# Kernel tuning notes

Hardware: AMD Instinct MI355X
Metric: run time of the kernel (lower is better)

## Reference

```python
import jax, jax.numpy as jnp
import numpy as np

HIDDEN_DIM = 128
NUM_HEADS = 4
B, S = 16, 1024
NEG = -1e9
EPS = 1e-5


def setup_inputs() -> dict:
    key = jax.random.key(0)
    ks = jax.random.split(key, 6)
    D, H = HIDDEN_DIM, NUM_HEADS
    x = jax.random.normal(ks[0], (B, S, D), dtype=jnp.float32)
    edge_type_matrix = jax.random.randint(ks[1], (S, S), 0, 5, dtype=jnp.int64)
    scale = 0.02
    W_in = jax.random.normal(ks[2], (H, 3 * D, D), dtype=jnp.float32) * scale   # per-head in_proj_weight
    b_in = jax.random.normal(ks[3], (H, 3 * D), dtype=jnp.float32) * scale      # per-head in_proj_bias
    W_out = jax.random.normal(ks[4], (H, D, D), dtype=jnp.float32) * scale      # per-head out_proj.weight
    b_out = jax.random.normal(ks[5], (H, D), dtype=jnp.float32) * scale         # per-head out_proj.bias
    return {"x": x, "edge_type_matrix": edge_type_matrix,
            "W_in": W_in, "b_in": b_in, "W_out": W_out, "b_out": b_out}


def reference(x, edge_type_matrix, W_in, b_in, W_out, b_out):
    Bx, Sx, D = x.shape
    H = W_in.shape[0]
    # F.layer_norm(x, x.size()[1:]): normalize jointly over (S, D), no affine
    mu = jnp.mean(x, axis=(1, 2), keepdims=True)
    var = jnp.mean(jnp.square(x - mu), axis=(1, 2), keepdims=True)
    xn = (x - mu) / jnp.sqrt(var + EPS)
    # all heads' qkv in one contraction: [b,h,s,3D]
    qkv = jnp.einsum('bsd,hed->bhse', xn, W_in) + b_in[None, :, None, :]
    q, k, v = jnp.split(qkv, 3, axis=-1)                      # each [b,h,s,D]
    scores = jnp.einsum('bhsd,bhtd->bhst', q, k) / jnp.sqrt(jnp.float32(D))
    # additive mask per head: 0 where edge_type == head_id(1..H), else -1e9
    head_ids = jnp.arange(1, H + 1, dtype=edge_type_matrix.dtype)
    mask = jnp.where(edge_type_matrix[None, :, :] == head_ids[:, None, None],
                     jnp.float32(0.0), jnp.float32(NEG))       # [h,s,s]
    attn = jax.nn.softmax(scores + mask[None], axis=-1)
    ctx = jnp.einsum('bhst,bhtd->bhsd', attn, v)
    # torch out_proj: ctx @ W.T + b
    out_h = jnp.einsum('bhsd,hed->bhse', ctx, W_out) + b_out[None, :, None, :]
    # dropout p=0.05 is identity in eval mode; concat heads on feature dim
    out = jnp.transpose(out_h, (0, 2, 1, 3)).reshape(Bx, Sx, H * D)
    return out


if __name__ == '__main__':
    inp = setup_inputs()
    y = reference(**inp)
    print(y.shape)
```

## Files before the change

kernel.cpp:

```cpp
#include <hip/hip_runtime.h>
#include <math.h>

static constexpr int Dh = 128;
static constexpr int NH = 4;
static constexpr int NB = 16;
static constexpr int SS = 1024;
static constexpr float NEGF = -1e9f;
static constexpr float SCALE = 0.08838834764831843f;

typedef short s16x8 __attribute__((ext_vector_type(8)));
typedef short s16x4 __attribute__((ext_vector_type(4)));
typedef float f32x4 __attribute__((ext_vector_type(4)));

#define MFMA32(a, b, c) __builtin_amdgcn_mfma_f32_16x16x32_bf16(a, b, c, 0, 0, 0)
#define MFMA16(a, b, c) __builtin_amdgcn_mfma_f32_16x16x16bf16_1k(a, b, c, 0, 0, 0)

#define GL2LDS16(g, l)                                                                   \
    __builtin_amdgcn_global_load_lds((const __attribute__((address_space(1))) void*)(g), \
                                     (__attribute__((address_space(3))) void*)(l), 16, 0, 0)

__device__ inline ushort f2bf(float f) {
    union { float f; unsigned u; } v; v.f = f;
    unsigned r = v.u + 0x7FFFu + ((v.u >> 16) & 1u);
    return (ushort)(r >> 16);
}

__global__ __launch_bounds__(256) void ln_mask_kernel(const float* __restrict__ x,
                                                      float* __restrict__ part,
                                                      const int* __restrict__ edge,
                                                      unsigned long long* __restrict__ mbit,
                                                      const float* __restrict__ w_in,
                                                      ushort* __restrict__ wb) {
    const int b = blockIdx.x >> 4, p = blockIdx.x & 15;
    const int tid = threadIdx.x;
    const float4* xb4 = (const float4*)(x + (size_t)b * SS * Dh) + p * 2048;
    float s = 0.f, ss = 0.f;
    for (int i = tid; i < 2048; i += 256) {
        float4 v = xb4[i];
        s  += v.x + v.y + v.z + v.w;
        ss += v.x * v.x + v.y * v.y + v.z * v.z + v.w * v.w;
    }
    __shared__ float r1[256], r2[256];
    r1[tid] = s; r2[tid] = ss;
    __syncthreads();
    for (int off = 128; off > 0; off >>= 1) {
        if (tid < off) { r1[tid] += r1[tid + off]; r2[tid] += r2[tid + off]; }
        __syncthreads();
    }
    if (tid == 0) { part[blockIdx.x * 2] = r1[0]; part[blockIdx.x * 2 + 1] = r2[0]; }

    if (blockIdx.x < 64) {
        const int idx = blockIdx.x * 256 + tid;
        const int sr = idx >> 4, w = idx & 15;
        const int4* ep = (const int4*)(edge + (size_t)sr * SS + w * 64);
        unsigned long long m0 = 0, m1 = 0, m2 = 0, m3 = 0;
        #pragma unroll
        for (int j = 0; j < 16; ++j) {
            int4 e = ep[j];
            const int base = j * 4;
            m0 |= (e.x == 1) ? (1ull << (base + 0)) : 0ull;
            m1 |= (e.x == 2) ? (1ull << (base + 0)) : 0ull;
            m2 |= (e.x == 3) ? (1ull << (base + 0)) : 0ull;
            m3 |= (e.x == 4) ? (1ull << (base + 0)) : 0ull;
            m0 |= (e.y == 1) ? (1ull << (base + 1)) : 0ull;
            m1 |= (e.y == 2) ? (1ull << (base + 1)) : 0ull;
            m2 |= (e.y == 3) ? (1ull << (base + 1)) : 0ull;
            m3 |= (e.y == 4) ? (1ull << (base + 1)) : 0ull;
            m0 |= (e.z == 1) ? (1ull << (base + 2)) : 0ull;
            m1 |= (e.z == 2) ? (1ull << (base + 2)) : 0ull;
            m2 |= (e.z == 3) ? (1ull << (base + 2)) : 0ull;
            m3 |= (e.z == 4) ? (1ull << (base + 2)) : 0ull;
            m0 |= (e.w == 1) ? (1ull << (base + 3)) : 0ull;
            m1 |= (e.w == 2) ? (1ull << (base + 3)) : 0ull;
            m2 |= (e.w == 3) ? (1ull << (base + 3)) : 0ull;
            m3 |= (e.w == 4) ? (1ull << (base + 3)) : 0ull;
        }
        mbit[((size_t)0 * SS + sr) * 16 + w] = m0;
        mbit[((size_t)1 * SS + sr) * 16 + w] = m1;
        mbit[((size_t)2 * SS + sr) * 16 + w] = m2;
        mbit[((size_t)3 * SS + sr) * 16 + w] = m3;
    } else if (blockIdx.x < 160) {
        const int slot = (blockIdx.x - 64) * 256 + tid;
        const float4* sp = (const float4*)w_in + (size_t)slot * 2;
        float4 a = sp[0], c = sp[1];
        s16x8 pk;
        pk[0] = (short)f2bf(a.x); pk[1] = (short)f2bf(a.y);
        pk[2] = (short)f2bf(a.z); pk[3] = (short)f2bf(a.w);
        pk[4] = (short)f2bf(c.x); pk[5] = (short)f2bf(c.y);
        pk[6] = (short)f2bf(c.z); pk[7] = (short)f2bf(c.w);
        *(s16x8*)(wb + (size_t)slot * 8) = pk;
    }
}

__global__ __launch_bounds__(256) void xcast_kernel(const float* __restrict__ x,
                                                    const float* __restrict__ part,
                                                    ushort* __restrict__ xb) {
    const int b = blockIdx.x >> 6;
    float s = 0.f, ss = 0.f;
    #pragma unroll
    for (int p = 0; p < 16; ++p) { s += part[(b * 16 + p) * 2]; ss += part[(b * 16 + p) * 2 + 1]; }
    const float invN = 1.0f / (float)(SS * Dh);
    const float mu = s * invN;
    const float rstd = 1.0f / sqrtf(ss * invN - mu * mu + 1e-5f);
    const size_t base = ((size_t)blockIdx.x * 256 + threadIdx.x) * 8;
    float4 v0 = *(const float4*)(x + base);
    float4 v1 = *(const float4*)(x + base + 4);
    s16x8 pk;
    pk[0] = (short)f2bf((v0.x - mu) * rstd); pk[1] = (short)f2bf((v0.y - mu) * rstd);
    pk[2] = (short)f2bf((v0.z - mu) * rstd); pk[3] = (short)f2bf((v0.w - mu) * rstd);
    pk[4] = (short)f2bf((v1.x - mu) * rstd); pk[5] = (short)f2bf((v1.y - mu) * rstd);
    pk[6] = (short)f2bf((v1.z - mu) * rstd); pk[7] = (short)f2bf((v1.w - mu) * rstd);
    *(s16x8*)(xb + base) = pk;
}

__global__ __launch_bounds__(256) void qkv_mfma_kernel(const ushort* __restrict__ xb,
                                                       const ushort* __restrict__ wb,
                                                       const float* __restrict__ bias,
                                                       ushort* __restrict__ qo,
                                                       ushort* __restrict__ ko,
                                                       ushort* __restrict__ vto) {
    __shared__ ushort smem[2 * 128 * 72];
    ushort* As = smem;
    ushort* Bs = smem + 128 * 72;
    ushort* Rs = smem;
    const int tid = threadIdx.x, wave = tid >> 6, lane = tid & 63;
    const int lrow = lane & 15, quad = lane >> 4;
    const int wm = wave & 1, wn = wave >> 1;
    const int col0 = blockIdx.x * 128;
    const int row0 = blockIdx.y * 128;
    const int bb = row0 >> 10;

    f32x4 acc[4][4];
    #pragma unroll
    for (int mi = 0; mi < 4; ++mi)
        #pragma unroll
        for (int ni = 0; ni < 4; ++ni) acc[mi][ni] = (f32x4){0.f, 0.f, 0.f, 0.f};

    for (int kk = 0; kk < 128; kk += 64) {
        if (kk) __syncthreads();
        #pragma unroll
        for (int p = 0; p < 4; ++p) {
            int slot = p * 256 + tid;
            int r = slot >> 3, c8 = (slot & 7) * 8;
            *(s16x8*)&As[r * 72 + c8] = *(const s16x8*)(xb + (size_t)(row0 + r) * Dh + kk + c8);
            *(s16x8*)&Bs[r * 72 + c8] = *(const s16x8*)(wb + (size_t)(col0 + r) * Dh + kk + c8);
        }
        __syncthreads();
        #pragma unroll
        for (int kc = 0; kc < 2; ++kc) {
            s16x8 af[4], bf[4];
            #pragma unroll
            for (int mi = 0; mi < 4; ++mi)
                af[mi] = *(const s16x8*)&As[(wm * 64 + 16 * mi + lrow) * 72 + kc * 32 + quad * 8];
            #pragma unroll
            for (int ni = 0; ni < 4; ++ni)
                bf[ni] = *(const s16x8*)&Bs[(wn * 64 + 16 * ni + lrow) * 72 + kc * 32 + quad * 8];
            #pragma unroll
            for (int mi = 0; mi < 4; ++mi)
                #pragma unroll
                for (int ni = 0; ni < 4; ++ni)
                    acc[mi][ni] = MFMA32(af[mi], bf[ni], acc[mi][ni]);
        }
    }

    const int seg = col0 % 384, typ = seg >> 7, h = col0 / 384;
    const size_t bh = (size_t)bb * NH + h;
    const int sl_blk = row0 & 1023;
    float bia[4];
    #pragma unroll
    for (int ni = 0; ni < 4; ++ni) bia[ni] = bias[col0 + wn * 64 + 16 * ni + lrow];
    const float sc = (typ == 0) ? SCALE : 1.f;

    __syncthreads();
    if (typ < 2) {
        #pragma unroll
        for (int mi = 0; mi < 4; ++mi)
            #pragma unroll
            for (int ni = 0; ni < 4; ++ni)
                #pragma unroll
                for (int reg = 0; reg < 4; ++reg)
                    Rs[(wm * 64 + 16 * mi + quad * 4 + reg) * 136 + wn * 64 + 16 * ni + lrow]
                        = f2bf((acc[mi][ni][reg] + bia[ni]) * sc);
    } else {
        #pragma unroll
        for (int mi = 0; mi < 4; ++mi)
            #pragma unroll
            for (int ni = 0; ni < 4; ++ni) {
                ushort4 pk;
                pk.x = f2bf(acc[mi][ni][0] + bia[ni]);
                pk.y = f2bf(acc[mi][ni][1] + bia[ni]);
                pk.z = f2bf(acc[mi][ni][2] + bia[ni]);
                pk.w = f2bf(acc[mi][ni][3] + bia[ni]);
                *(ushort4*)&Rs[(wn * 64 + 16 * ni + lrow) * 136 + wm * 64 + 16 * mi + quad * 4] = pk;
            }
    }
    __syncthreads();

    ushort* dstb;
    int pitch;
    if (typ == 0)      { dstb = qo  + bh * SS * 128 + (size_t)sl_blk * 128; pitch = 128; }
    else if (typ == 1) { dstb = ko  + bh * SS * 128 + (size_t)sl_blk * 128; pitch = 128; }
    else               { dstb = vto + bh * (size_t)128 * SS + sl_blk;       pitch = SS;  }
    #pragma unroll
    for (int p = 0; p < 8; ++p) {
        int slot = p * 256 + tid;
        int r = slot >> 4, c8 = (slot & 15) * 8;
        *(s16x8*)&dstb[(size_t)r * pitch + c8] = *(const s16x8*)&Rs[r * 136 + c8];
    }
}

static constexpr int KSW = 128;
static constexpr int VSW = 64;
static constexpr int TILE_U = 64 * KSW + 128 * VSW;
static constexpr int WS_LD = 136;
static constexpr int OS_LD = 136;

__global__ __launch_bounds__(256, 2) void attn_fused_kernel(const ushort* __restrict__ qg_,
                                                            const ushort* __restrict__ kg_,
                                                            const ushort* __restrict__ vg_,
                                                            const unsigned long long* __restrict__ mbit,
                                                            const float* __restrict__ wo,
                                                            const float* __restrict__ bo,
                                                            float* __restrict__ out) {
    const int bhi = blockIdx.x, qt = blockIdx.y;
    const int b = bhi >> 2, h = bhi & 3;
    const int s0 = qt * 128;
    const int tid = threadIdx.x;
    const int wave = tid >> 6, lane = tid & 63;
    const int lrow = lane & 15, quad = lane >> 4;

    __shared__ ushort smem[2 * TILE_U];
    ushort* Osl = smem + wave * 16 * OS_LD;
    ushort* Ws  = smem + 4 * 16 * OS_LD;

    const size_t bh = (size_t)(b * NH + h);
    const ushort* qg = qg_ + bh * SS * 128;
    const ushort* kg = kg_ + bh * SS * 128;
    const ushort* vg = vg_ + bh * 128 * SS;
    const unsigned long long* mrow0 = mbit + ((size_t)h * SS + (s0 + 32 * wave + lrow)) * 16;
    const unsigned long long* mrow1 = mrow0 + 16 * 16;

    s16x8 qf[2][4];
    #pragma unroll
    for (int g = 0; g < 2; ++g) {
        const ushort* qr = qg + (size_t)(s0 + 32 * wave + 16 * g + lrow) * 128 + quad * 8;
        #pragma unroll
        for (int kc = 0; kc < 4; ++kc) qf[g][kc] = *(const s16x8*)(qr + kc * 32);
    }

    #define ISSUE_TILE(T0, KD, VD)                                                            \
        {                                                                                     \
            _Pragma("unroll")                                                                 \
            for (int p = 0; p < 4; ++p) {                                                     \
                const int rk = wave * 16 + p * 4 + (lane >> 4);                               \
                GL2LDS16(kg + (size_t)((T0) + rk) * 128 + (((lane & 15) * 8) ^ ((rk & 7) << 3)), \
                         (KD) + (wave * 16 + p * 4) * KSW);                                   \
                const int rv = wave * 32 + p * 8 + (lane >> 3);                               \
                GL2LDS16(vg + (size_t)rv * SS + (T0) + (((lane & 7) * 8) ^ ((rv & 7) << 3)),  \
                         (VD) + (wave * 32 + p * 8) * VSW);                                   \
            }                                                                                 \
        }

    ISSUE_TILE(0, smem, smem + 64 * KSW);

    f32x4 oacc[2][8];
    #pragma unroll
    for (int g = 0; g < 2; ++g)
        #pragma unroll
        for (int nb = 0; nb < 8; ++nb) oacc[g][nb] = (f32x4){0.f, 0.f, 0.f, 0.f};
    float m_run[2] = {-INFINITY, -INFINITY};
    float l_run[2] = {0.f, 0.f};

    for (int kt = 0; kt < 16; ++kt) {
        const ushort* Ksc = smem + (kt & 1) * TILE_U;
        const ushort* Vtc = Ksc + 64 * KSW;

        __syncthreads();

        if (kt < 15) {
            ushort* Ksn = smem + ((kt + 1) & 1) * TILE_U;
            ISSUE_TILE((kt + 1) * 64, Ksn, Ksn + 64 * KSW);
        }
        const unsigned long long mw0 = mrow0[kt];
        const unsigned long long mw1 = mrow1[kt];

        f32x4 sacc[2][4];
        #pragma unroll
        for (int g = 0; g < 2; ++g)
            #pragma unroll
            for (int cb = 0; cb < 4; ++cb) sacc[g][cb] = (f32x4){0.f, 0.f, 0.f, 0.f};
        #pragma unroll
        for (int cb = 0; cb < 4; ++cb) {
            s16x8 kf[4];
            #pragma unroll
            for (int kc = 0; kc < 4; ++kc)
                kf[kc] = *(const s16x8*)&Ksc[(16 * cb + lrow) * KSW
                                             + ((kc * 32 + quad * 8) ^ ((lrow & 7) << 3))];
            #pragma unroll
            for (int g = 0; g < 2; ++g)
                #pragma unroll
                for (int kc = 0; kc < 4; ++kc)
                    sacc[g][cb] = MFMA32(kf[kc], qf[g][kc], sacc[g][cb]);
        }

        s16x4 pf[2][4];
        #pragma unroll
        for (int g = 0; g < 2; ++g) {
            const unsigned long long mw = g ? mw1 : mw0;
            float sv[4][4];
            float tm = -INFINITY;
            #pragma unroll
            for (int cb = 0; cb < 4; ++cb) {
                unsigned nib = (unsigned)(mw >> (16 * cb + quad * 4)) & 0xFu;
                #pragma unroll
                for (int r = 0; r < 4; ++r) {
                    sv[cb][r] = (nib & (1u << r)) ? sacc[g][cb][r] : NEGF;
                    tm = fmaxf(tm, sv[cb][r]);
                }
            }
            tm = fmaxf(tm, __shfl_xor(tm, 16));
            tm = fmaxf(tm, __shfl_xor(tm, 32));
            float mn = fmaxf(m_run[g], tm);
            float al = __expf(m_run[g] - mn);
            float rs = 0.f;
            #pragma unroll
            for (int cb = 0; cb < 4; ++cb) {
                float p0 = __expf(sv[cb][0] - mn);
                float p1 = __expf(sv[cb][1] - mn);
                float p2 = __expf(sv[cb][2] - mn);
                float p3 = __expf(sv[cb][3] - mn);
                rs += (p0 + p1) + (p2 + p3);
                s16x4 pk;
                pk[0] = (short)f2bf(p0); pk[1] = (short)f2bf(p1);
                pk[2] = (short)f2bf(p2); pk[3] = (short)f2bf(p3);
                pf[g][cb] = pk;
            }
            rs += __shfl_xor(rs, 16);
            rs += __shfl_xor(rs, 32);
            l_run[g] = l_run[g] * al + rs;
            m_run[g] = mn;
            #pragma unroll
            for (int nb = 0; nb < 8; ++nb)
                #pragma unroll
                for (int r = 0; r < 4; ++r) oacc[g][nb][r] *= al;
        }

        #pragma unroll
        for (int nb = 0; nb < 8; ++nb) {
            #pragma unroll
            for (int kb = 0; kb < 4; ++kb) {
                s16x4 vf = *(const s16x4*)&Vtc[(16 * nb + lrow) * VSW
                                               + ((kb * 16 + quad * 4) ^ ((lrow & 7) << 3))];
                #pragma unroll
                for (int g = 0; g < 2; ++g)
                    oacc[g][nb] = MFMA16(vf, pf[g][kb], oacc[g][nb]);
            }
        }
    }
    #undef ISSUE_TILE

    __syncthreads();
    const float* wbase = wo + (size_t)h * Dh * Dh;
    #pragma unroll
    for (int p = 0; p < 16; ++p) {
        int slot = p * 256 + tid;
        int r = slot >> 5, c4 = (slot & 31) << 2;
        float4 wv = *(const float4*)(wbase + (size_t)r * Dh + c4);
        ushort4 pb;
        pb.x = f2bf(wv.x); pb.y = f2bf(wv.y); pb.z = f2bf(wv.z); pb.w = f2bf(wv.w);
        *(ushort4*)&Ws[r * WS_LD + c4] = pb;
    }
    s16x8 afo[2][4];
    #pragma unroll
    for (int g = 0; g < 2; ++g) {
        float inv = 1.0f / l_run[g];
        #pragma unroll
        for (int nb = 0; nb < 8; ++nb) {
            ushort4 pk;
            pk.x = f2bf(oacc[g][nb][0] * inv);
            pk.y = f2bf(oacc[g][nb][1] * inv);
            pk.z = f2bf(oacc[g][nb][2] * inv);
            pk.w = f2bf(oacc[g][nb][3] * inv);
            *(ushort4*)&Osl[lrow * OS_LD + 16 * nb + quad * 4] = pk;
        }
        #pragma unroll
        for (int kc = 0; kc < 4; ++kc)
            afo[g][kc] = *(const s16x8*)&Osl[lrow * OS_LD + kc * 32 + quad * 8];
    }
    __syncthreads();

    const size_t orow0 = (size_t)b * SS + s0 + 32 * wave;
    #pragma unroll
    for (int nb = 0; nb < 8; ++nb) {
        float bia = bo[h * Dh + nb * 16 + lrow];
        f32x4 facc[2];
        facc[0] = (f32x4){0.f, 0.f, 0.f, 0.f};
        facc[1] = (f32x4){0.f, 0.f, 0.f, 0.f};
        #pragma unroll
        for (int kc = 0; kc < 4; ++kc) {
            s16x8 wf = *(const s16x8*)&Ws[(16 * nb + lrow) * WS_LD + kc * 32 + quad * 8];
            facc[0] = MFMA32(afo[0][kc], wf, facc[0]);
            facc[1] = MFMA32(afo[1][kc], wf, facc[1]);
        }
        #pragma unroll
        for (int g = 0; g < 2; ++g)
            #pragma unroll
            for (int reg = 0; reg < 4; ++reg) {
                size_t m = orow0 + 16 * g + quad * 4 + reg;
                out[m * (NH * Dh) + h * Dh + nb * 16 + lrow] = facc[g][reg] + bia;
            }
    }
}

extern "C" void kernel_launch(void* const* d_in, const int* in_sizes, int n_in,
                              void* d_out, int out_size, void* d_ws, size_t ws_size,
                              hipStream_t stream) {
    const float* x     = (const float*)d_in[0];
    const int*   edge  = (const int*)d_in[1];
    const float* w_in  = (const float*)d_in[2];
    const float* b_in  = (const float*)d_in[3];
    const float* w_out = (const float*)d_in[4];
    const float* b_out = (const float*)d_in[5];
    float* out = (float*)d_out;

    float* ws   = (float*)d_ws;
    float* part = ws;
    unsigned long long* mbit = (unsigned long long*)(ws + 1024);
    ushort* qo  = (ushort*)(mbit + (size_t)NH * SS * 16);
    const size_t QSZ = (size_t)NB * NH * SS * 128;
    ushort* ko  = qo + QSZ;
    ushort* vto = ko + QSZ;
    ushort* xb  = vto + QSZ;
    ushort* wb  = xb + (size_t)NB * SS * Dh;

    ln_mask_kernel<<<256, 256, 0, stream>>>(x, part, edge, mbit, w_in, wb);
    xcast_kernel<<<1024, 256, 0, stream>>>(x, part, xb);
    qkv_mfma_kernel<<<dim3(12, 128), 256, 0, stream>>>(xb, wb, b_in, qo, ko, vto);
    attn_fused_kernel<<<dim3(NB * NH, SS / 128), 256, 0, stream>>>(qo, ko, vto, mbit, w_out, b_out, out);
}
```

Baseline: 160.3 us.

## Fuse layer-norm cast into QKV GEMM and load operands directly from global

Removes the separate xcast kernel. The QKV GEMM now reads fp32 x straight from global memory, normalizes it with the per-batch statistics and converts it to bf16 in registers. It also drops LDS staging of the A and B tiles, loading MFMA fragments directly from global memory. This saves a launch and the bf16 round trip through memory. In exchange, each of the 12 column blocks re-reads and re-normalizes the same fp32 rows, and the fragment loads from global are less coalesced.

```diff
diff --git a/kernel.cpp b/kernel.cpp
--- a/kernel.cpp
+++ b/kernel.cpp
@@ -92,37 +92,14 @@
     }
 }
 
-__global__ __launch_bounds__(256) void xcast_kernel(const float* __restrict__ x,
-                                                    const float* __restrict__ part,
-                                                    ushort* __restrict__ xb) {
-    const int b = blockIdx.x >> 6;
-    float s = 0.f, ss = 0.f;
-    #pragma unroll
-    for (int p = 0; p < 16; ++p) { s += part[(b * 16 + p) * 2]; ss += part[(b * 16 + p) * 2 + 1]; }
-    const float invN = 1.0f / (float)(SS * Dh);
-    const float mu = s * invN;
-    const float rstd = 1.0f / sqrtf(ss * invN - mu * mu + 1e-5f);
-    const size_t base = ((size_t)blockIdx.x * 256 + threadIdx.x) * 8;
-    float4 v0 = *(const float4*)(x + base);
-    float4 v1 = *(const float4*)(x + base + 4);
-    s16x8 pk;
-    pk[0] = (short)f2bf((v0.x - mu) * rstd); pk[1] = (short)f2bf((v0.y - mu) * rstd);
-    pk[2] = (short)f2bf((v0.z - mu) * rstd); pk[3] = (short)f2bf((v0.w - mu) * rstd);
-    pk[4] = (short)f2bf((v1.x - mu) * rstd); pk[5] = (short)f2bf((v1.y - mu) * rstd);
-    pk[6] = (short)f2bf((v1.z - mu) * rstd); pk[7] = (short)f2bf((v1.w - mu) * rstd);
-    *(s16x8*)(xb + base) = pk;
-}
-
-__global__ __launch_bounds__(256) void qkv_mfma_kernel(const ushort* __restrict__ xb,
+__global__ __launch_bounds__(256) void qkv_mfma_kernel(const float* __restrict__ x,
+                                                       const float* __restrict__ part,
                                                        const ushort* __restrict__ wb,
                                                        const float* __restrict__ bias,
                                                        ushort* __restrict__ qo,
                                                        ushort* __restrict__ ko,
                                                        ushort* __restrict__ vto) {
-    __shared__ ushort smem[2 * 128 * 72];
-    ushort* As = smem;
-    ushort* Bs = smem + 128 * 72;
-    ushort* Rs = smem;
+    __shared__ ushort Rs[128 * 136];
     const int tid = threadIdx.x, wave = tid >> 6, lane = tid & 63;
     const int lrow = lane & 15, quad = lane >> 4;
     const int wm = wave & 1, wn = wave >> 1;
@@ -130,37 +107,42 @@
     const int row0 = blockIdx.y * 128;
     const int bb = row0 >> 10;
 
+    float s_ = 0.f, ss_ = 0.f;
+    #pragma unroll
+    for (int p = 0; p < 16; ++p) { s_ += part[(bb * 16 + p) * 2]; ss_ += part[(bb * 16 + p) * 2 + 1]; }
+    const float invN = 1.0f / (float)(SS * Dh);
+    const float mu = s_ * invN;
+    const float rstd = 1.0f / sqrtf(ss_ * invN - mu * mu + 1e-5f);
+
     f32x4 acc[4][4];
     #pragma unroll
     for (int mi = 0; mi < 4; ++mi)
         #pragma unroll
         for (int ni = 0; ni < 4; ++ni) acc[mi][ni] = (f32x4){0.f, 0.f, 0.f, 0.f};
 
-    for (int kk = 0; kk < 128; kk += 64) {
-        if (kk) __syncthreads();
-        #pragma unroll
-        for (int p = 0; p < 4; ++p) {
-            int slot = p * 256 + tid;
-            int r = slot >> 3, c8 = (slot & 7) * 8;
-            *(s16x8*)&As[r * 72 + c8] = *(const s16x8*)(xb + (size_t)(row0 + r) * Dh + kk + c8);
-            *(s16x8*)&Bs[r * 72 + c8] = *(const s16x8*)(wb + (size_t)(col0 + r) * Dh + kk + c8);
-        }
-        __syncthreads();
-        #pragma unroll
-        for (int kc = 0; kc < 2; ++kc) {
-            s16x8 af[4], bf[4];
-            #pragma unroll
-            for (int mi = 0; mi < 4; ++mi)
-                af[mi] = *(const s16x8*)&As[(wm * 64 + 16 * mi + lrow) * 72 + kc * 32 + quad * 8];
+    #pragma unroll
+    for (int kc = 0; kc < 4; ++kc) {
+        s16x8 af[4], bf[4];
+        #pragma unroll
+        for (int mi = 0; mi < 4; ++mi) {
+            const float* ap = x + (size_t)(row0 + wm * 64 + 16 * mi + lrow) * Dh + kc * 32 + quad * 8;
+            float4 a0 = *(const float4*)ap;
+            float4 a1 = *(const float4*)(ap + 4);
+            s16x8 pa;
+            pa[0] = (short)f2bf((a0.x - mu) * rstd); pa[1] = (short)f2bf((a0.y - mu) * rstd);
+            pa[2] = (short)f2bf((a0.z - mu) * rstd); pa[3] = (short)f2bf((a0.w - mu) * rstd);
+            pa[4] = (short)f2bf((a1.x - mu) * rstd); pa[5] = (short)f2bf((a1.y - mu) * rstd);
+            pa[6] = (short)f2bf((a1.z - mu) * rstd); pa[7] = (short)f2bf((a1.w - mu) * rstd);
+            af[mi] = pa;
+        }
+        #pragma unroll
+        for (int ni = 0; ni < 4; ++ni)
+            bf[ni] = *(const s16x8*)(wb + (size_t)(col0 + wn * 64 + 16 * ni + lrow) * Dh + kc * 32 + quad * 8);
+        #pragma unroll
+        for (int mi = 0; mi < 4; ++mi)
             #pragma unroll
             for (int ni = 0; ni < 4; ++ni)
-                bf[ni] = *(const s16x8*)&Bs[(wn * 64 + 16 * ni + lrow) * 72 + kc * 32 + quad * 8];
-            #pragma unroll
-            for (int mi = 0; mi < 4; ++mi)
-                #pragma unroll
-                for (int ni = 0; ni < 4; ++ni)
-                    acc[mi][ni] = MFMA32(af[mi], bf[ni], acc[mi][ni]);
-        }
+                acc[mi][ni] = MFMA32(af[mi], bf[ni], acc[mi][ni]);
     }
 
     const int seg = col0 % 384, typ = seg >> 7, h = col0 / 384;
@@ -171,7 +153,6 @@
     for (int ni = 0; ni < 4; ++ni) bia[ni] = bias[col0 + wn * 64 + 16 * ni + lrow];
     const float sc = (typ == 0) ? SCALE : 1.f;
 
-    __syncthreads();
     if (typ < 2) {
         #pragma unroll
         for (int mi = 0; mi < 4; ++mi)
@@ -430,11 +411,9 @@
     const size_t QSZ = (size_t)NB * NH * SS * 128;
     ushort* ko  = qo + QSZ;
     ushort* vto = ko + QSZ;
-    ushort* xb  = vto + QSZ;
-    ushort* wb  = xb + (size_t)NB * SS * Dh;
+    ushort* wb  = vto + QSZ;
 
     ln_mask_kernel<<<256, 256, 0, stream>>>(x, part, edge, mbit, w_in, wb);
-    xcast_kernel<<<1024, 256, 0, stream>>>(x, part, xb);
-    qkv_mfma_kernel<<<dim3(12, 128), 256, 0, stream>>>(xb, wb, b_in, qo, ko, vto);
+    qkv_mfma_kernel<<<dim3(12, 128), 256, 0, stream>>>(x, part, wb, b_in, qo, ko, vto);
     attn_fused_kernel<<<dim3(NB * NH, SS / 128), 256, 0, stream>>>(qo, ko, vto, mbit, w_out, b_out, out);
 }
```

After: 178.1 us. 11.1% more time.
